# Kernel tuning notes

Measured on AMD Instinct MI355X. Metric: run time of the kernel, lower is better.

Reference implementation:

```python
import jax, jax.numpy as jnp
import numpy as np

NEG_INF = -1e9  # large negative used to mask the H-direction self position (CCNet INF trick)


def _cca(x, q_w, q_b, k_w, k_b, v_w, v_b, gamma):
    # x: [B, C, H, W]
    B, C, H, W = x.shape
    # 1x1 convs are per-pixel channel matmuls
    q = jnp.einsum('oc,bchw->bohw', q_w, x) + q_b[None, :, None, None]  # [B,2,H,W]
    k = jnp.einsum('oc,bchw->bohw', k_w, x) + k_b[None, :, None, None]  # [B,2,H,W]
    v = jnp.einsum('oc,bchw->bohw', v_w, x) + v_b[None, :, None, None]  # [B,16,H,W]

    # column (H-direction) affinities: query (h,w) vs keys (j,w)
    energy_H = jnp.einsum('bchw,bcjw->bhwj', q, k)  # [B,H,W,H]
    diag = jnp.eye(H, dtype=bool)[None, :, None, :]  # mask j == h (self counted once, in W branch)
    energy_H = jnp.where(diag, NEG_INF, energy_H)
    # row (W-direction) affinities: query (h,w) vs keys (h,j)
    energy_W = jnp.einsum('bchw,bchj->bhwj', q, k)  # [B,H,W,W]

    attn = jax.nn.softmax(jnp.concatenate([energy_H, energy_W], axis=3), axis=3)  # [B,H,W,H+W]
    att_H = attn[..., :H]
    att_W = attn[..., H:]

    out_H = jnp.einsum('bhwj,bcjw->bchw', att_H, v)
    out_W = jnp.einsum('bhwj,bchj->bchw', att_W, v)
    return gamma[0] * (out_H + out_W) + x


def setup_inputs() -> dict:
    key = jax.random.key(0)
    ks = jax.random.split(key, 8)
    b, c, d, h, w = 1, 16, 24, 96, 192
    return {
        'cost_volume': jax.random.normal(ks[0], (b, c, d, h, w), jnp.float32),
        'q_w': jax.random.normal(ks[1], (2, 16), jnp.float32) * 0.1,
        'q_b': jax.random.normal(ks[2], (2,), jnp.float32) * 0.1,
        'k_w': jax.random.normal(ks[3], (2, 16), jnp.float32) * 0.1,
        'k_b': jax.random.normal(ks[4], (2,), jnp.float32) * 0.1,
        'v_w': jax.random.normal(ks[5], (16, 16), jnp.float32) * 0.1,
        'v_b': jax.random.normal(ks[6], (16,), jnp.float32) * 0.1,
        'gamma': jax.random.normal(ks[7], (1,), jnp.float32),
    }


def reference(cost_volume, q_w, q_b, k_w, k_b, v_w, v_b, gamma):
    b, c, d, h, w = cost_volume.shape
    # fold disparity into batch: [b,c,d,h,w] -> [b*d, c, h, w]
    x = jnp.transpose(cost_volume, (0, 2, 1, 3, 4)).reshape(b * d, c, h, w)
    x = _cca(x, q_w, q_b, k_w, k_b, v_w, v_b, gamma)
    x = _cca(x, q_w, q_b, k_w, k_b, v_w, v_b, gamma)  # same module applied twice
    return jnp.transpose(x.reshape(b, d, c, h, w), (0, 2, 1, 3, 4))
```

## Files before the change

kernel.cpp:

```cpp
#include <hip/hip_runtime.h>

#define C 16
#define NIMG 24
#define H 96
#define W 192
#define PX (H*W)
#define LOG2E 1.44269504088896f

typedef float v2f  __attribute__((ext_vector_type(2)));
typedef float v4f  __attribute__((ext_vector_type(4)));
typedef short v8s  __attribute__((ext_vector_type(8)));

#define QP_OFF 0
#define KP_OFF (NIMG*PX*2)
#define VP_OFF (2*NIMG*PX*2)
#define CMAX_OFF (VP_OFF + NIMG*PX*C)
#define RMAX_OFF (CMAX_OFF + NIMG*2*W)
#define SC_OFF   (RMAX_OFF + NIMG*2*H)
#define ACC_OFF  (SC_OFF + NIMG*PX)

__device__ __forceinline__ short f2bf(float x) {
    union { float f; unsigned u; } v; v.f = x;
    unsigned r = v.u + 0x7fffu + ((v.u >> 16) & 1u);
    return (short)(r >> 16);
}
__device__ __forceinline__ float bf2f(unsigned short u) {
    union { unsigned u; float f; } v; v.u = ((unsigned)u) << 16;
    return v.f;
}

__global__ __launch_bounds__(256)
void qkv_kernel(const float* __restrict__ x, long xn_s, long xc_s,
                const float* __restrict__ qw, const float* __restrict__ qb,
                const float* __restrict__ kw, const float* __restrict__ kb,
                const float* __restrict__ vw, const float* __restrict__ vb,
                float2* __restrict__ Qp, float2* __restrict__ Kp,
                float4* __restrict__ Vp)
{
    __shared__ float wq[2*C+2], wk[2*C+2], wv[C*C+C];
    int tid = threadIdx.x;
    if (tid < 2*C) { wq[tid] = qw[tid]; wk[tid] = kw[tid]; }
    if (tid < 2)   { wq[2*C+tid] = qb[tid]; wk[2*C+tid] = kb[tid]; }
    if (tid < C*C) wv[tid] = vw[tid];
    if (tid < C)   wv[C*C+tid] = vb[tid];
    __syncthreads();

    int id = blockIdx.x*256 + tid;
    int n  = id / PX;
    int p  = id - n*PX;
    int h  = p / W;
    int w  = p - h*W;
    const float* xp = x + (long)n*xn_s + p;

    float xv[C];
    #pragma unroll
    for (int c = 0; c < C; c++) xv[c] = xp[(long)c*xc_s];

    float q0 = wq[2*C], q1 = wq[2*C+1];
    float k0 = wk[2*C], k1 = wk[2*C+1];
    #pragma unroll
    for (int c = 0; c < C; c++) {
        q0 += wq[c]*xv[c];   q1 += wq[C+c]*xv[c];
        k0 += wk[c]*xv[c];   k1 += wk[C+c]*xv[c];
    }
    Qp[id] = make_float2(q0, q1);
    Kp[id] = make_float2(k0, k1);

    float vv[C];
    #pragma unroll
    for (int o = 0; o < C; o++) {
        float a = wv[C*C+o];
        #pragma unroll
        for (int c = 0; c < C; c++) a += wv[o*C+c]*xv[c];
        vv[o] = a;
    }
    #pragma unroll
    for (int c4 = 0; c4 < 4; c4++)
        Vp[(((long)n*H + h)*4 + c4)*W + w] =
            make_float4(vv[c4*4+0], vv[c4*4+1], vv[c4*4+2], vv[c4*4+3]);
}

__global__ __launch_bounds__(192)
void stats_kernel(const float2* __restrict__ Kp,
                  float* __restrict__ cmax, float* __restrict__ rmax)
{
    int n = blockIdx.x;
    int tid = threadIdx.x;
    const float2* Kpn = Kp + n*PX;

    float c0 = 0.f, c1 = 0.f;
    for (int h = 0; h < H; h++) {
        float2 k = Kpn[h*W + tid];
        c0 = fmaxf(c0, fabsf(k.x));
        c1 = fmaxf(c1, fabsf(k.y));
    }
    cmax[n*2*W + tid]     = c0;
    cmax[n*2*W + W + tid] = c1;

    if (tid < H) {
        float r0 = 0.f, r1 = 0.f;
        for (int j = 0; j < W; j++) {
            float2 k = Kpn[tid*W + j];
            r0 = fmaxf(r0, fabsf(k.x));
            r1 = fmaxf(r1, fabsf(k.y));
        }
        rmax[n*2*H + tid]     = r0;
        rmax[n*2*H + H + tid] = r1;
    }
}

#define VT_WS 1672
__global__ __launch_bounds__(256)
void col_attn_kernel(const float2* __restrict__ Qp, const float2* __restrict__ Kp,
                     const v4f* __restrict__ Vp,
                     const float* __restrict__ cmax, const float* __restrict__ rmax,
                     unsigned short* __restrict__ accC, float* __restrict__ sC)
{
    __shared__ unsigned short Vt[4*VT_WS];
    __shared__ unsigned short Ks[4*2*96];
    __shared__ float2         Qs[4*96];
    __shared__ float          Ms[4*96];

    const int chunk = (NIMG*48) / 8;
    int bid = blockIdx.x;
    int swz = (bid & 7)*chunk + (bid >> 3);
    int n   = swz / 48;
    int wg  = swz - n*48;
    int w0  = wg*4;
    int tid = threadIdx.x;

    const float2* Qpn = Qp + n*PX;
    const float2* Kpn = Kp + n*PX;
    const v4f*    Vpn = Vp + (long)n*PX*4;

    #pragma unroll
    for (int i = 0; i < 6; i++) {
        int idx = i*256 + tid;
        int wl  = idx & 3;
        int c4  = (idx >> 2) & 3;
        int j   = idx >> 4;
        v4f v = Vpn[((long)j*4 + c4)*W + w0 + wl];
        int b = wl*VT_WS + (c4*4)*104 + j;
        Vt[b        ] = (unsigned short)f2bf(v[0]);
        Vt[b + 104  ] = (unsigned short)f2bf(v[1]);
        Vt[b + 208  ] = (unsigned short)f2bf(v[2]);
        Vt[b + 312  ] = (unsigned short)f2bf(v[3]);
    }
    #pragma unroll
    for (int i = 0; i < 2; i++) {
        int idx = i*256 + tid;
        if (idx < 384) {
            int wl = idx & 3;
            int j  = idx >> 2;
            float2 kk = Kpn[j*W + w0 + wl];
            Ks[wl*192 + j]      = (unsigned short)f2bf(kk.x);
            Ks[wl*192 + 96 + j] = (unsigned short)f2bf(kk.y);
        }
    }
    #pragma unroll
    for (int i = 0; i < 2; i++) {
        int idx = i*256 + tid;
        if (idx < 384) {
            int wl = idx & 3;
            int h  = idx >> 2;
            int w  = w0 + wl;
            float2 qq = Qpn[h*W + w];
            float qx = qq.x * LOG2E, qy = qq.y * LOG2E;
            float c0 = cmax[n*2*W + w], c1 = cmax[n*2*W + W + w];
            float r0 = rmax[n*2*H + h], r1 = rmax[n*2*H + H + h];
            float ax = fabsf(qx), ay = fabsf(qy);
            Qs[wl*96 + h] = make_float2(qx, qy);
            Ms[wl*96 + h] = fmaxf(ax*c0 + ay*c1, ax*r0 + ay*r1);
        }
    }
    __syncthreads();

    int wl   = tid >> 6;
    int lane = tid & 63;
    int li   = lane & 15;
    int g    = lane >> 4;
    int w    = w0 + wl;
    unsigned short* accCn = accC + (long)n*PX*16;

    #pragma unroll
    for (int ht = 0; ht < 6; ht++) {
        int hglob = ht*16 + li;
        float2 q = Qs[wl*96 + hglob];
        float  m = Ms[wl*96 + hglob];

        v4f acc = {};
        float sp = 0.f;
        #pragma unroll
        for (int kc = 0; kc < 3; kc++) {
            int j0 = kc*32 + g*8;
            v8s bv = *(const v8s*)&Vt[wl*VT_WS + li*104 + j0];
            v8s kxv = *(const v8s*)&Ks[wl*192 + j0];
            v8s kyv = *(const v8s*)&Ks[wl*192 + 96 + j0];
            v8s af;
            #pragma unroll
            for (int e = 0; e < 8; e++) {
                float e2 = bf2f((unsigned short)kxv[e])*q.x
                         + bf2f((unsigned short)kyv[e])*q.y - m;
                float p = __builtin_amdgcn_exp2f(e2);
                p = (j0 + e == hglob) ? 0.0f : p;
                sp += p;
                af[e] = f2bf(p);
            }
            acc = __builtin_amdgcn_mfma_f32_16x16x32_bf16(af, bv, acc, 0, 0, 0);
        }
        sp += __shfl_xor(sp, 16);
        sp += __shfl_xor(sp, 32);
        if (lane < 16)
            sC[((long)n*H + hglob)*W + w] = sp;

        #pragma unroll
        for (int rr = 0; rr < 4; rr++) {
            int h2 = ht*16 + g*4 + rr;
            accCn[((long)h2*W + w)*16 + li] = (unsigned short)f2bf(acc[rr]);
        }
    }
}

__global__ __launch_bounds__(256)
void row_attn_kernel(const float2* __restrict__ Qp, const float2* __restrict__ Kp,
                     const v4f* __restrict__ Vp,
                     const float* __restrict__ cmax, const float* __restrict__ rmax,
                     const unsigned short* __restrict__ accC, const float* __restrict__ sC,
                     const float* __restrict__ xres, long xn_s, long xc_s,
                     float* __restrict__ out, long on_s, long oc_s,
                     const float* __restrict__ gamma_p)
{
    __shared__ __align__(16) unsigned short Vl[2][16][200];
    __shared__ __align__(16) float          Kl[2][192][2];

    const int chunk = (NIMG*(H/2)) / 8;
    int bid = blockIdx.x;
    int swz = (bid & 7)*chunk + (bid >> 3);
    int n   = swz / (H/2);
    int h0  = (swz - n*(H/2)) * 2;
    int tid = threadIdx.x;

    const float2* Qpn = Qp + n*PX;
    const float2* Kpn = Kp + n*PX;
    const v4f*    Vpn = Vp + (long)n*PX*4;

    #pragma unroll
    for (int i = 0; i < 6; i++) {
        int idx = i*256 + tid;
        int rr  = idx / 768;
        int rem = idx - rr*768;
        int c4  = rem / 192;
        int w2  = rem - c4*192;
        v4f v = Vpn[((long)(h0+rr)*4 + c4)*W + w2];
        Vl[rr][c4*4+0][w2] = (unsigned short)f2bf(v[0]);
        Vl[rr][c4*4+1][w2] = (unsigned short)f2bf(v[1]);
        Vl[rr][c4*4+2][w2] = (unsigned short)f2bf(v[2]);
        Vl[rr][c4*4+3][w2] = (unsigned short)f2bf(v[3]);
    }
    if (tid < 192) {
        float2 ka = Kpn[(h0+0)*W + tid];
        float2 kb = Kpn[(h0+1)*W + tid];
        Kl[0][tid][0] = ka.x;  Kl[0][tid][1] = ka.y;
        Kl[1][tid][0] = kb.x;  Kl[1][tid][1] = kb.y;
    }

    int wv   = tid >> 6;
    int r    = wv >> 1;
    int half = wv & 1;
    int lane = tid & 63;
    int li   = lane & 15;
    int g    = lane >> 4;
    int h    = h0 + r;

    float r0 = rmax[n*2*H + h], r1 = rmax[n*2*H + H + h];
    float qx[6], qy[6], mW[6];
    #pragma unroll
    for (int t = 0; t < 6; t++) {
        int w = (half*6 + t)*16 + li;
        float2 qq = Qpn[h*W + w];
        float c0 = cmax[n*2*W + w], c1 = cmax[n*2*W + W + w];
        float lqx = qq.x * LOG2E, lqy = qq.y * LOG2E;
        qx[t] = lqx; qy[t] = lqy;
        mW[t] = fmaxf(fabsf(lqx)*c0 + fabsf(lqy)*c1, fabsf(lqx)*r0 + fabsf(lqy)*r1);
    }

    __syncthreads();

    v4f acc[6] = {};
    float sp[6] = {0.f,0.f,0.f,0.f,0.f,0.f};

    #pragma unroll
    for (int kc = 0; kc < 6; kc++) {
        int j0 = kc*32 + g*8;
        v8s af = *(const v8s*)&Vl[r][li][j0];
        const v4f* kp4 = (const v4f*)&Kl[r][j0][0];
        v4f k0 = kp4[0], k1 = kp4[1], k2 = kp4[2], k3 = kp4[3];
        float kxv[8] = {k0[0],k0[2],k1[0],k1[2],k2[0],k2[2],k3[0],k3[2]};
        float kyv[8] = {k0[1],k0[3],k1[1],k1[3],k2[1],k2[3],k3[1],k3[3]};
        #pragma unroll
        for (int t = 0; t < 6; t++) {
            v8s bf;
            float sl = sp[t];
            #pragma unroll
            for (int e = 0; e < 8; e++) {
                float ev = qx[t]*kxv[e] + qy[t]*kyv[e];
                float p = __builtin_amdgcn_exp2f(ev - mW[t]);
                sl += p;
                bf[e] = f2bf(p);
            }
            sp[t] = sl;
            acc[t] = __builtin_amdgcn_mfma_f32_16x16x32_bf16(af, bf, acc[t], 0, 0, 0);
        }
    }

    float gam = gamma_p[0];
    #pragma unroll
    for (int t = 0; t < 6; t++) {
        float s = sp[t];
        s += __shfl_xor(s, 16);
        s += __shfl_xor(s, 32);
        int w = (half*6 + t)*16 + li;
        float st = sC[((long)n*H + h)*W + w] + s;
        float inv = 1.0f / st;
        long po = (long)h*W + w;
        const unsigned short* cap = accC + (((long)n*H + h)*W + w)*16 + g*4;
        #pragma unroll
        for (int rr = 0; rr < 4; rr++) {
            int c = g*4 + rr;
            float ac = bf2f(cap[rr]);
            float tot = (acc[t][rr] + ac) * inv;
            out[(long)n*on_s + (long)c*oc_s + po] =
                gam*tot + xres[(long)n*xn_s + (long)c*xc_s + po];
        }
    }
}

extern "C" void kernel_launch(void* const* d_in, const int* in_sizes, int n_in,
                              void* d_out, int out_size, void* d_ws, size_t ws_size,
                              hipStream_t stream) {
    const float* cost = (const float*)d_in[0];
    const float* q_w  = (const float*)d_in[1];
    const float* q_b  = (const float*)d_in[2];
    const float* k_w  = (const float*)d_in[3];
    const float* k_b  = (const float*)d_in[4];
    const float* v_w  = (const float*)d_in[5];
    const float* v_b  = (const float*)d_in[6];
    const float* gamma= (const float*)d_in[7];
    float* out = (float*)d_out;
    float* ws  = (float*)d_ws;

    float2* Qp = (float2*)(ws + QP_OFF);
    float2* Kp = (float2*)(ws + KP_OFF);
    float4* Vp = (float4*)(ws + VP_OFF);
    float*  cm = ws + CMAX_OFF;
    float*  rm = ws + RMAX_OFF;
    float*  sC = ws + SC_OFF;
    unsigned short* aC = (unsigned short*)(ws + ACC_OFF);

    const int qkv_blocks = (NIMG*PX)/256;
    const int col_blocks = NIMG*48;
    const int row_blocks = NIMG*(H/2);

    qkv_kernel<<<qkv_blocks, 256, 0, stream>>>(
        cost, (long)PX, (long)NIMG*PX,
        q_w, q_b, k_w, k_b, v_w, v_b, Qp, Kp, Vp);
    stats_kernel<<<NIMG, 192, 0, stream>>>(Kp, cm, rm);
    col_attn_kernel<<<col_blocks, 256, 0, stream>>>(
        Qp, Kp, (const v4f*)Vp, cm, rm, aC, sC);
    row_attn_kernel<<<row_blocks, 256, 0, stream>>>(
        Qp, Kp, (const v4f*)Vp, cm, rm, aC, sC,
        cost, (long)PX, (long)NIMG*PX,
        out,  (long)PX, (long)NIMG*PX,
        gamma);

    qkv_kernel<<<qkv_blocks, 256, 0, stream>>>(
        out, (long)PX, (long)NIMG*PX,
        q_w, q_b, k_w, k_b, v_w, v_b, Qp, Kp, Vp);
    stats_kernel<<<NIMG, 192, 0, stream>>>(Kp, cm, rm);
    col_attn_kernel<<<col_blocks, 256, 0, stream>>>(
        Qp, Kp, (const v4f*)Vp, cm, rm, aC, sC);
    row_attn_kernel<<<row_blocks, 256, 0, stream>>>(
        Qp, Kp, (const v4f*)Vp, cm, rm, aC, sC,
        out, (long)PX, (long)NIMG*PX,
        out, (long)PX, (long)NIMG*PX,
        gamma);
}
```

Baseline: 166.3 us.

## Store V as bf16 in two layouts, parallelize stats, drop row-kernel LDS staging

The QKV kernel now converts V to bf16 once and writes it in two layouts: a ushort4-packed layout for the column kernel and a planar per-channel layout for the row kernel. This halves V traffic and removes the repeated float-to-bf16 conversions in the attention kernels. The row kernel now reads V and K directly from global memory instead of staging them in LDS, which also drops a barrier. The stats kernel is split across four blocks per image, using atomicMax on the float bit patterns (valid because the values are non-negative), with the column max buffer zeroed inside the QKV kernel. In exchange, the QKV kernel does more writes and the row kernel relies on cache for reuse instead of LDS.

```diff
diff --git a/kernel.cpp b/kernel.cpp
--- a/kernel.cpp
+++ b/kernel.cpp
@@ -13,16 +13,17 @@
 
 #define QP_OFF 0
 #define KP_OFF (NIMG*PX*2)
-#define VP_OFF (2*NIMG*PX*2)
-#define CMAX_OFF (VP_OFF + NIMG*PX*C)
+#define VB4_OFF (2*NIMG*PX*2)
+#define VBP_OFF (VB4_OFF + NIMG*PX*C/2)
+#define CMAX_OFF (VBP_OFF + NIMG*PX*C/2)
 #define RMAX_OFF (CMAX_OFF + NIMG*2*W)
 #define SC_OFF   (RMAX_OFF + NIMG*2*H)
 #define ACC_OFF  (SC_OFF + NIMG*PX)
 
-__device__ __forceinline__ short f2bf(float x) {
+__device__ __forceinline__ unsigned short f2bf(float x) {
     union { float f; unsigned u; } v; v.f = x;
     unsigned r = v.u + 0x7fffu + ((v.u >> 16) & 1u);
-    return (short)(r >> 16);
+    return (unsigned short)(r >> 16);
 }
 __device__ __forceinline__ float bf2f(unsigned short u) {
     union { unsigned u; float f; } v; v.u = ((unsigned)u) << 16;
@@ -35,7 +36,8 @@
                 const float* __restrict__ kw, const float* __restrict__ kb,
                 const float* __restrict__ vw, const float* __restrict__ vb,
                 float2* __restrict__ Qp, float2* __restrict__ Kp,
-                float4* __restrict__ Vp)
+                ushort4* __restrict__ Vb4, unsigned short* __restrict__ Vbp,
+                float* __restrict__ cmax_zero)
 {
     __shared__ float wq[2*C+2], wk[2*C+2], wv[C*C+C];
     int tid = threadIdx.x;
@@ -43,6 +45,11 @@
     if (tid < 2)   { wq[2*C+tid] = qb[tid]; wk[2*C+tid] = kb[tid]; }
     if (tid < C*C) wv[tid] = vw[tid];
     if (tid < C)   wv[C*C+tid] = vb[tid];
+
+    if (blockIdx.x < 36) {
+        int zi = blockIdx.x*256 + tid;
+        if (zi < NIMG*2*W) cmax_zero[zi] = 0.0f;
+    }
     __syncthreads();
 
     int id = blockIdx.x*256 + tid;
@@ -74,45 +81,63 @@
         for (int c = 0; c < C; c++) a += wv[o*C+c]*xv[c];
         vv[o] = a;
     }
-    #pragma unroll
-    for (int c4 = 0; c4 < 4; c4++)
-        Vp[(((long)n*H + h)*4 + c4)*W + w] =
-            make_float4(vv[c4*4+0], vv[c4*4+1], vv[c4*4+2], vv[c4*4+3]);
+    unsigned short vb16[C];
+    #pragma unroll
+    for (int o = 0; o < C; o++) vb16[o] = f2bf(vv[o]);
+
+    #pragma unroll
+    for (int c4 = 0; c4 < 4; c4++) {
+        ushort4 u;
+        u.x = vb16[c4*4+0]; u.y = vb16[c4*4+1];
+        u.z = vb16[c4*4+2]; u.w = vb16[c4*4+3];
+        Vb4[(((long)n*H + h)*4 + c4)*W + w] = u;
+    }
+    #pragma unroll
+    for (int o = 0; o < C; o++)
+        Vbp[(((long)n*H + h)*16 + o)*W + w] = vb16[o];
 }
 
 __global__ __launch_bounds__(192)
 void stats_kernel(const float2* __restrict__ Kp,
                   float* __restrict__ cmax, float* __restrict__ rmax)
 {
-    int n = blockIdx.x;
+    int bid = blockIdx.x;
+    int n   = bid >> 2;
+    int h0  = (bid & 3) * 24;
     int tid = threadIdx.x;
     const float2* Kpn = Kp + n*PX;
 
     float c0 = 0.f, c1 = 0.f;
-    for (int h = 0; h < H; h++) {
-        float2 k = Kpn[h*W + tid];
+    #pragma unroll 4
+    for (int h = 0; h < 24; h++) {
+        float2 k = Kpn[(h0+h)*W + tid];
         c0 = fmaxf(c0, fabsf(k.x));
         c1 = fmaxf(c1, fabsf(k.y));
     }
-    cmax[n*2*W + tid]     = c0;
-    cmax[n*2*W + W + tid] = c1;
-
-    if (tid < H) {
-        float r0 = 0.f, r1 = 0.f;
-        for (int j = 0; j < W; j++) {
-            float2 k = Kpn[tid*W + j];
-            r0 = fmaxf(r0, fabsf(k.x));
-            r1 = fmaxf(r1, fabsf(k.y));
-        }
-        rmax[n*2*H + tid]     = r0;
-        rmax[n*2*H + H + tid] = r1;
+    atomicMax((unsigned*)&cmax[n*2*W + tid],     __float_as_uint(c0));
+    atomicMax((unsigned*)&cmax[n*2*W + W + tid], __float_as_uint(c1));
+
+    int r = tid >> 3, seg = tid & 7;
+    float r0 = 0.f, r1 = 0.f;
+    const float2* kr = Kpn + (h0+r)*W + seg*24;
+    #pragma unroll 4
+    for (int j = 0; j < 24; j++) {
+        float2 k = kr[j];
+        r0 = fmaxf(r0, fabsf(k.x));
+        r1 = fmaxf(r1, fabsf(k.y));
+    }
+    r0 = fmaxf(r0, __shfl_xor(r0, 1)); r0 = fmaxf(r0, __shfl_xor(r0, 2)); r0 = fmaxf(r0, __shfl_xor(r0, 4));
+    r1 = fmaxf(r1, __shfl_xor(r1, 1)); r1 = fmaxf(r1, __shfl_xor(r1, 2)); r1 = fmaxf(r1, __shfl_xor(r1, 4));
+    if (seg == 0) {
+        rmax[n*2*H + h0 + r]     = r0;
+        rmax[n*2*H + H + h0 + r] = r1;
     }
 }
 
 #define VT_WS 1672
 __global__ __launch_bounds__(256)
 void col_attn_kernel(const float2* __restrict__ Qp, const float2* __restrict__ Kp,
-                     const v4f* __restrict__ Vp,
+                     const ushort4* __restrict__ Vb4,
                      const float* __restrict__ cmax, const float* __restrict__ rmax,
                      unsigned short* __restrict__ accC, float* __restrict__ sC)
 {
@@ -131,7 +156,7 @@
 
     const float2* Qpn = Qp + n*PX;
     const float2* Kpn = Kp + n*PX;
-    const v4f*    Vpn = Vp + (long)n*PX*4;
+    const ushort4* Vbn = Vb4 + (long)n*PX*4;
 
     #pragma unroll
     for (int i = 0; i < 6; i++) {
@@ -139,12 +164,12 @@
         int wl  = idx & 3;
         int c4  = (idx >> 2) & 3;
         int j   = idx >> 4;
-        v4f v = Vpn[((long)j*4 + c4)*W + w0 + wl];
+        ushort4 v = Vbn[((long)j*4 + c4)*W + w0 + wl];
         int b = wl*VT_WS + (c4*4)*104 + j;
-        Vt[b        ] = (unsigned short)f2bf(v[0]);
-        Vt[b + 104  ] = (unsigned short)f2bf(v[1]);
-        Vt[b + 208  ] = (unsigned short)f2bf(v[2]);
-        Vt[b + 312  ] = (unsigned short)f2bf(v[3]);
+        Vt[b        ] = v.x;
+        Vt[b + 104  ] = v.y;
+        Vt[b + 208  ] = v.z;
+        Vt[b + 312  ] = v.w;
     }
     #pragma unroll
     for (int i = 0; i < 2; i++) {
@@ -153,8 +178,8 @@
             int wl = idx & 3;
             int j  = idx >> 2;
             float2 kk = Kpn[j*W + w0 + wl];
-            Ks[wl*192 + j]      = (unsigned short)f2bf(kk.x);
-            Ks[wl*192 + 96 + j] = (unsigned short)f2bf(kk.y);
+            Ks[wl*192 + j]      = f2bf(kk.x);
+            Ks[wl*192 + 96 + j] = f2bf(kk.y);
         }
     }
     #pragma unroll
@@ -204,7 +229,7 @@
                 float p = __builtin_amdgcn_exp2f(e2);
                 p = (j0 + e == hglob) ? 0.0f : p;
                 sp += p;
-                af[e] = f2bf(p);
+                af[e] = (short)f2bf(p);
             }
             acc = __builtin_amdgcn_mfma_f32_16x16x32_bf16(af, bv, acc, 0, 0, 0);
         }
@@ -216,23 +241,20 @@
         #pragma unroll
         for (int rr = 0; rr < 4; rr++) {
             int h2 = ht*16 + g*4 + rr;
-            accCn[((long)h2*W + w)*16 + li] = (unsigned short)f2bf(acc[rr]);
+            accCn[((long)h2*W + w)*16 + li] = f2bf(acc[rr]);
         }
     }
 }
 
 __global__ __launch_bounds__(256)
 void row_attn_kernel(const float2* __restrict__ Qp, const float2* __restrict__ Kp,
-                     const v4f* __restrict__ Vp,
+                     const unsigned short* __restrict__ Vbp,
                      const float* __restrict__ cmax, const float* __restrict__ rmax,
                      const unsigned short* __restrict__ accC, const float* __restrict__ sC,
                      const float* __restrict__ xres, long xn_s, long xc_s,
                      float* __restrict__ out, long on_s, long oc_s,
                      const float* __restrict__ gamma_p)
 {
-    __shared__ __align__(16) unsigned short Vl[2][16][200];
-    __shared__ __align__(16) float          Kl[2][192][2];
-
     const int chunk = (NIMG*(H/2)) / 8;
     int bid = blockIdx.x;
     int swz = (bid & 7)*chunk + (bid >> 3);
@@ -241,28 +263,8 @@
     int tid = threadIdx.x;
 
     const float2* Qpn = Qp + n*PX;
-    const float2* Kpn = Kp + n*PX;
-    const v4f*    Vpn = Vp + (long)n*PX*4;
-
-    #pragma unroll
-    for (int i = 0; i < 6; i++) {
-        int idx = i*256 + tid;
-        int rr  = idx / 768;
-        int rem = idx - rr*768;
-        int c4  = rem / 192;
-        int w2  = rem - c4*192;
-        v4f v = Vpn[((long)(h0+rr)*4 + c4)*W + w2];
-        Vl[rr][c4*4+0][w2] = (unsigned short)f2bf(v[0]);
-        Vl[rr][c4*4+1][w2] = (unsigned short)f2bf(v[1]);
-        Vl[rr][c4*4+2][w2] = (unsigned short)f2bf(v[2]);
-        Vl[rr][c4*4+3][w2] = (unsigned short)f2bf(v[3]);
-    }
-    if (tid < 192) {
-        float2 ka = Kpn[(h0+0)*W + tid];
-        float2 kb = Kpn[(h0+1)*W + tid];
-        Kl[0][tid][0] = ka.x;  Kl[0][tid][1] = ka.y;
-        Kl[1][tid][0] = kb.x;  Kl[1][tid][1] = kb.y;
-    }
+    const float*  Kf  = (const float*)(Kp + n*PX);
+    const unsigned short* Vrn = Vbp + (long)n*PX*16;
 
     int wv   = tid >> 6;
     int r    = wv >> 1;
@@ -284,16 +286,17 @@
         mW[t] = fmaxf(fabsf(lqx)*c0 + fabsf(lqy)*c1, fabsf(lqx)*r0 + fabsf(lqy)*r1);
     }
 
-    __syncthreads();
-
     v4f acc[6] = {};
     float sp[6] = {0.f,0.f,0.f,0.f,0.f,0.f};
 
+    const unsigned short* Vrow = Vrn + (long)h*16*W + (long)li*W;
+    const float*          Krow = Kf + (long)h*W*2;
+
     #pragma unroll
     for (int kc = 0; kc < 6; kc++) {
         int j0 = kc*32 + g*8;
-        v8s af = *(const v8s*)&Vl[r][li][j0];
-        const v4f* kp4 = (const v4f*)&Kl[r][j0][0];
+        v8s af = *(const v8s*)(Vrow + j0);
+        const v4f* kp4 = (const v4f*)(Krow + j0*2);
         v4f k0 = kp4[0], k1 = kp4[1], k2 = kp4[2], k3 = kp4[3];
         float kxv[8] = {k0[0],k0[2],k1[0],k1[2],k2[0],k2[2],k3[0],k3[2]};
         float kyv[8] = {k0[1],k0[3],k1[1],k1[3],k2[1],k2[3],k3[1],k3[3]};
@@ -306,7 +309,7 @@
                 float ev = qx[t]*kxv[e] + qy[t]*kyv[e];
                 float p = __builtin_amdgcn_exp2f(ev - mW[t]);
                 sl += p;
-                bf[e] = f2bf(p);
+                bf[e] = (short)f2bf(p);
             }
             sp[t] = sl;
             acc[t] = __builtin_amdgcn_mfma_f32_16x16x32_bf16(af, bf, acc[t], 0, 0, 0);
@@ -349,38 +352,40 @@
     float* out = (float*)d_out;
     float* ws  = (float*)d_ws;
 
-    float2* Qp = (float2*)(ws + QP_OFF);
-    float2* Kp = (float2*)(ws + KP_OFF);
-    float4* Vp = (float4*)(ws + VP_OFF);
-    float*  cm = ws + CMAX_OFF;
-    float*  rm = ws + RMAX_OFF;
-    float*  sC = ws + SC_OFF;
+    float2*  Qp = (float2*)(ws + QP_OFF);
+    float2*  Kp = (float2*)(ws + KP_OFF);
+    ushort4* Vb4 = (ushort4*)(ws + VB4_OFF);
+    unsigned short* Vbp = (unsigned short*)(ws + VBP_OFF);
+    float*   cm = ws + CMAX_OFF;
+    float*   rm = ws + RMAX_OFF;
+    float*   sC = ws + SC_OFF;
     unsigned short* aC = (unsigned short*)(ws + ACC_OFF);
 
-    const int qkv_blocks = (NIMG*PX)/256;
-    const int col_blocks = NIMG*48;
-    const int row_blocks = NIMG*(H/2);
+    const int qkv_blocks  = (NIMG*PX)/256;
+    const int stat_blocks = NIMG*4;
+    const int col_blocks  = NIMG*48;
+    const int row_blocks  = NIMG*(H/2);
 
     qkv_kernel<<<qkv_blocks, 256, 0, stream>>>(
         cost, (long)PX, (long)NIMG*PX,
-        q_w, q_b, k_w, k_b, v_w, v_b, Qp, Kp, Vp);
-    stats_kernel<<<NIMG, 192, 0, stream>>>(Kp, cm, rm);
+        q_w, q_b, k_w, k_b, v_w, v_b, Qp, Kp, Vb4, Vbp, cm);
+    stats_kernel<<<stat_blocks, 192, 0, stream>>>(Kp, cm, rm);
     col_attn_kernel<<<col_blocks, 256, 0, stream>>>(
-        Qp, Kp, (const v4f*)Vp, cm, rm, aC, sC);
+        Qp, Kp, Vb4, cm, rm, aC, sC);
     row_attn_kernel<<<row_blocks, 256, 0, stream>>>(
-        Qp, Kp, (const v4f*)Vp, cm, rm, aC, sC,
+        Qp, Kp, Vbp, cm, rm, aC, sC,
         cost, (long)PX, (long)NIMG*PX,
         out,  (long)PX, (long)NIMG*PX,
         gamma);
 
     qkv_kernel<<<qkv_blocks, 256, 0, stream>>>(
         out, (long)PX, (long)NIMG*PX,
-        q_w, q_b, k_w, k_b, v_w, v_b, Qp, Kp, Vp);
-    stats_kernel<<<NIMG, 192, 0, stream>>>(Kp, cm, rm);
+        q_w, q_b, k_w, k_b, v_w, v_b, Qp, Kp, Vb4, Vbp, cm);
+    stats_kernel<<<stat_blocks, 192, 0, stream>>>(Kp, cm, rm);
     col_attn_kernel<<<col_blocks, 256, 0, stream>>>(
-        Qp, Kp, (const v4f*)Vp, cm, rm, aC, sC);
+        Qp, Kp, Vb4, cm, rm, aC, sC);
     row_attn_kernel<<<row_blocks, 256, 0, stream>>>(
-        Qp, Kp, (const v4f*)Vp, cm, rm, aC, sC,
+        Qp, Kp, Vbp, cm, rm, aC, sC,
         out, (long)PX, (long)NIMG*PX,
         out, (long)PX, (long)NIMG*PX,
         gamma);
```

Measured after the change: 156.3 us. 1.06x faster.
